# Optimization experiments

Hardware: AMD Instinct MI355X
Metric: run time of the kernel (lower is better)

Reference implementation:

```python
import jax, jax.numpy as jnp
import numpy as np

N_EXPERTS = 8
TOP_K = 2


def setup_inputs() -> dict:
    key = jax.random.key(0)
    ks = jax.random.split(key, 5)
    B, T, C, E, H = 8, 2048, 256, 8, 682  # H = int(8/3*256)
    scale = 1.0 / np.sqrt(C)
    return {
        "x": jax.random.normal(ks[0], (B, T, C), dtype=jnp.float32),
        "router_w": jax.random.normal(ks[1], (E, C), dtype=jnp.float32) * scale,
        "w1": jax.random.normal(ks[2], (E, H, C), dtype=jnp.float32) * scale,
        "w2": jax.random.normal(ks[3], (E, C, H), dtype=jnp.float32) * (1.0 / np.sqrt(H)),
        "w3": jax.random.normal(ks[4], (E, H, C), dtype=jnp.float32) * scale,
    }


def reference(x, router_w, w1, w2, w3):
    B, T, C = x.shape
    flat = x.reshape(-1, C)  # [N, C]

    # Router: softmax over experts, top-k selection, renormalize.
    logits = flat @ router_w.T                     # [N, E]
    probs = jax.nn.softmax(logits, axis=-1)
    topk_probs, topk_idx = jax.lax.top_k(probs, TOP_K)
    topk_probs = topk_probs / (jnp.sum(topk_probs, axis=-1, keepdims=True) + 1e-9)

    # Dense gate matrix [N, E]: zero for non-selected experts (same math as
    # the masked loop, since unselected experts contribute weight 0).
    onehot = jax.nn.one_hot(topk_idx, N_EXPERTS, dtype=flat.dtype)  # [N, K, E]
    gates = jnp.einsum("nk,nke->ne", topk_probs, onehot)           # [N, E]

    # SwiGLU experts, computed densely over E and combined with gates.
    h1 = jnp.einsum("nc,ehc->neh", flat, w1)       # [N, E, H]
    h3 = jnp.einsum("nc,ehc->neh", flat, w3)       # [N, E, H]
    h = jax.nn.silu(h1) * h3                       # [N, E, H]
    y = jnp.einsum("neh,ech->nec", h, w2)          # [N, E, C]
    out = jnp.einsum("ne,nec->nc", gates, y)       # [N, C]
    return out.reshape(B, T, C)
```

## Files before the change

### kernel.cpp

```cpp
#include <hip/hip_runtime.h>
#include <hip/hip_bf16.h>

#define N_TOK 16384
#define C_DIM 256
#define E_NUM 8
#define H_DIM 682
#define H_PAD 768
#define NROWS (N_TOK * 2)
#define HB 64
#define APB (NROWS / HB)
#define MAXTILE 264

typedef short short8 __attribute__((ext_vector_type(8)));
typedef float floatx4 __attribute__((ext_vector_type(4)));
typedef unsigned int uint;

__device__ inline unsigned short f2bf(float v) {
    union { float f; uint u; } x; x.f = v;
    uint r = (x.u + 0x7fffu + ((x.u >> 16) & 1u)) >> 16;
    return (unsigned short)r;
}
__device__ inline float bf2f(unsigned short v) {
    union { uint u; float f; } x; x.u = ((uint)v) << 16; return x.f;
}
__device__ inline uint pk2(float a, float b) {
    return (uint)f2bf(a) | ((uint)f2bf(b) << 16);
}

__device__ __forceinline__ void load_lds16(const void* g, void* l) {
    __builtin_amdgcn_global_load_lds(
        (const __attribute__((address_space(1))) unsigned int*)g,
        (__attribute__((address_space(3))) unsigned int*)l, 16, 0, 0);
}

#define VMCNT8 asm volatile("s_waitcnt vmcnt(8)" ::: "memory")
#define VMCNT6 asm volatile("s_waitcnt vmcnt(6)" ::: "memory")
#define VMCNT0 asm volatile("s_waitcnt vmcnt(0)" ::: "memory")
#define LGKM0  asm volatile("s_waitcnt lgkmcnt(0)" ::: "memory")

#define P13 (E_NUM * H_PAD * (C_DIM / 2))
#define P2  (E_NUM * C_DIM * (H_PAD / 2))
#define NQUAD ((2 * P13 + P2) / 4)
#define WCONV_BLKS (NQUAD / 256)
#define Q13 (P13 / 4)

__global__ __launch_bounds__(256) void prep_kernel(
    const float* __restrict__ w1, const float* __restrict__ w3, const float* __restrict__ w2,
    unsigned short* __restrict__ w1b, unsigned short* __restrict__ w3b,
    unsigned short* __restrict__ w2b,
    const float* __restrict__ x, const float* __restrict__ rw,
    unsigned short* __restrict__ xb, int* __restrict__ as_e, float* __restrict__ as_gate) {
    __shared__ float rws[E_NUM * C_DIM];
    int tid = threadIdx.x;
    if (blockIdx.x < WCONV_BLKS) {
        int q = blockIdx.x * 256 + tid;
        if (q < 2 * Q13) {
            const float* src = (q < Q13) ? w1 : w3;
            unsigned short* dst = (q < Q13) ? w1b : w3b;
            int i4 = (q < Q13) ? q : q - Q13;
            int e = i4 / (H_PAD * 32);
            int rem = i4 - e * (H_PAD * 32);
            int r = rem >> 5;
            int qc = rem & 31;
            int4 v = {0, 0, 0, 0};
            if (r < H_DIM) {
                const float* s = src + ((size_t)e * H_DIM + r) * C_DIM + qc * 8;
                float4 f0 = *(const float4*)s;
                float4 f1 = *(const float4*)(s + 4);
                v.x = pk2(f0.x, f0.y); v.y = pk2(f0.z, f0.w);
                v.z = pk2(f1.x, f1.y); v.w = pk2(f1.z, f1.w);
            }
            *(int4*)((uint*)dst + (size_t)i4 * 4) = v;
        } else {
            int i4 = q - 2 * Q13;
            int e = i4 / (C_DIM * 96);
            int rem = i4 - e * (C_DIM * 96);
            int r = rem / 96;
            int qc = rem - r * 96;
            const float* s = w2 + ((size_t)e * C_DIM + r) * H_DIM;
            int4 v = {0, 0, 0, 0};
            int j0 = qc * 4;
#pragma unroll
            for (int k = 0; k < 4; k++) {
                int j = j0 + k;
                if (j * 2 < H_DIM) {
                    float2 f = *(const float2*)(s + j * 2);
                    ((uint*)&v)[k] = pk2(f.x, f.y);
                }
            }
            *(int4*)((uint*)w2b + (size_t)i4 * 4) = v;
        }
        return;
    }
    for (int i = tid; i < E_NUM * C_DIM; i += 256) rws[i] = rw[i];
    __syncthreads();
    int wave = tid >> 6, lane = tid & 63;
    int t = (blockIdx.x - WCONV_BLKS) * 4 + wave;
    const float4 xv = *(const float4*)(x + (size_t)t * C_DIM + lane * 4);
    uint2 pk;
    pk.x = pk2(xv.x, xv.y);
    pk.y = pk2(xv.z, xv.w);
    *(uint2*)(xb + (size_t)t * C_DIM + lane * 4) = pk;
    float p[E_NUM];
#pragma unroll
    for (int e = 0; e < E_NUM; e++) {
        const float* wr = &rws[e * C_DIM + lane * 4];
        p[e] = xv.x * wr[0] + xv.y * wr[1] + xv.z * wr[2] + xv.w * wr[3];
    }
#pragma unroll
    for (int off = 32; off >= 1; off >>= 1) {
#pragma unroll
        for (int e = 0; e < E_NUM; e++) p[e] += __shfl_down(p[e], off, 64);
    }
    if (lane == 0) {
        float m = p[0];
#pragma unroll
        for (int e = 1; e < E_NUM; e++) m = fmaxf(m, p[e]);
        float s = 0.f, q[E_NUM];
#pragma unroll
        for (int e = 0; e < E_NUM; e++) { q[e] = expf(p[e] - m); s += q[e]; }
#pragma unroll
        for (int e = 0; e < E_NUM; e++) q[e] /= s;
        int e0 = 0;
#pragma unroll
        for (int e = 1; e < E_NUM; e++) if (q[e] > q[e0]) e0 = e;
        int e1 = (e0 == 0) ? 1 : 0;
#pragma unroll
        for (int e = 0; e < E_NUM; e++) {
            if (e != e0 && q[e] > q[e1]) e1 = e;
        }
        float g0 = q[e0], g1 = q[e1];
        float denom = g0 + g1 + 1e-9f;
        g0 /= denom; g1 /= denom;
        as_e[t * 2] = e0; as_gate[t * 2] = g0;
        as_e[t * 2 + 1] = e1; as_gate[t * 2 + 1] = g1;
    }
}

__global__ __launch_bounds__(256) void hist_kernel(const int* __restrict__ as_e,
                                                   int* __restrict__ block_hist) {
    __shared__ int lh[E_NUM];
    int b = blockIdx.x, tid = threadIdx.x;
    if (tid < E_NUM) lh[tid] = 0;
    __syncthreads();
    for (int i = tid; i < APB; i += 256) atomicAdd(&lh[as_e[b * APB + i]], 1);
    __syncthreads();
    if (tid < E_NUM) block_hist[b * E_NUM + tid] = lh[tid];
}

__global__ void scan2_kernel(const int* __restrict__ block_hist, int* __restrict__ offsets,
                             int* __restrict__ block_base, int* __restrict__ tile_base) {
    __shared__ int tot[E_NUM], off[E_NUM];
    int e = threadIdx.x;
    if (e < E_NUM) {
        int s = 0;
        for (int b = 0; b < HB; b++) s += block_hist[b * E_NUM + e];
        tot[e] = s;
    }
    __syncthreads();
    if (e == 0) {
        int acc = 0;
        for (int i = 0; i < E_NUM; i++) { off[i] = acc; offsets[i] = acc; acc += tot[i]; }
        offsets[E_NUM] = acc;
        int t = 0;
        tile_base[0] = 0;
        for (int i = 0; i < E_NUM; i++) { t += (tot[i] + 127) / 128; tile_base[i + 1] = t; }
    }
    __syncthreads();
    if (e < E_NUM) {
        int acc = off[e];
        for (int b = 0; b < HB; b++) { block_base[b * E_NUM + e] = acc; acc += block_hist[b * E_NUM + e]; }
    }
}

__global__ __launch_bounds__(256) void scatter_kernel(
    const int* __restrict__ as_e, const int* __restrict__ block_base,
    int* __restrict__ row_token, int* __restrict__ as_row) {
    __shared__ int cur[E_NUM];
    int b = blockIdx.x, tid = threadIdx.x;
    if (tid < E_NUM) cur[tid] = block_base[b * E_NUM + tid];
    __syncthreads();
    for (int i = tid; i < APB; i += 256) {
        int a = b * APB + i;
        int e = as_e[a];
        int p = atomicAdd(&cur[e], 1);
        row_token[p] = a >> 1;
        as_row[a] = p;
    }
}

__device__ __forceinline__ int tile_to_expert(const int* __restrict__ tile_base, int bid) {
    int e = 0;
#pragma unroll
    for (int i = 1; i < E_NUM; i++) e += (bid >= tile_base[i]) ? 1 : 0;
    return e;
}

__global__ __launch_bounds__(256, 2) void expert_ffn1(
    const unsigned short* __restrict__ xb, const unsigned short* __restrict__ w1b,
    const unsigned short* __restrict__ w3b, const int* __restrict__ offsets,
    const int* __restrict__ tile_base, const int* __restrict__ row_token,
    unsigned short* __restrict__ h) {
    int bid = blockIdx.x;
    int xcd = bid & 7;
    int local = bid >> 3;
    int tq = local / 6;
    int c = local - tq * 6;
    int t = tq * 8 + xcd;
    if (t >= tile_base[E_NUM]) return;
    int e = tile_to_expert(tile_base, t);
    int mt = t - tile_base[e];
    int off0 = offsets[e], off1 = offsets[e + 1];
    int row0 = off0 + mt * 128;
    int mval = min(128, off1 - row0);

    __shared__ union {
        unsigned short buf[2][12288];
        unsigned short Hs[128 * 136];
    } sm;

    int tid = threadIdx.x, lane = tid & 63, w = tid >> 6;
    int wm = w & 1, wn = w >> 1;
    int ra = tid >> 2;
    int acol = (((tid & 3) ^ ((ra >> 1) & 3))) * 8;
    int tok0 = row_token[row0 + min(ra, mval - 1)];
    int tok1 = row_token[row0 + min(ra + 64, mval - 1)];
    const unsigned short* a0p = xb + (size_t)tok0 * C_DIM + acol;
    const unsigned short* a1p = xb + (size_t)tok1 * C_DIM + acol;
    const unsigned short* b1p0 = w1b + ((size_t)e * H_PAD + c * 128 + ra) * C_DIM + acol;
    const unsigned short* b1p1 = b1p0 + (size_t)64 * C_DIM;
    const unsigned short* b3p0 = w3b + ((size_t)e * H_PAD + c * 128 + ra) * C_DIM + acol;
    const unsigned short* b3p1 = b3p0 + (size_t)64 * C_DIM;

    int wofs = w * 512;
    auto stage = [&](int kt, unsigned short* base) {
        int kb = kt * 32;
        load_lds16(a0p + kb, base + wofs);
        load_lds16(a1p + kb, base + 2048 + wofs);
        load_lds16(b1p0 + kb, base + 4096 + wofs);
        load_lds16(b1p1 + kb, base + 6144 + wofs);
        load_lds16(b3p0 + kb, base + 8192 + wofs);
        load_lds16(b3p1 + kb, base + 10240 + wofs);
    };

    int ko = ((lane >> 4) ^ ((lane >> 1) & 3)) * 8;
    int l15 = lane & 15;
    int arowf = wm * 64 + l15;
    int browf = wn * 64 + l15;
    int quad = lane >> 4;

    stage(0, sm.buf[0]);

    floatx4 acc1[4][4], acc3[4][4];
#pragma unroll
    for (int m = 0; m < 4; m++)
#pragma unroll
        for (int n = 0; n < 4; n++) {
            acc1[m][n] = (floatx4){0.f, 0.f, 0.f, 0.f};
            acc3[m][n] = (floatx4){0.f, 0.f, 0.f, 0.f};
        }

#pragma unroll
    for (int kt = 0; kt < 8; kt++) {
        if (kt + 1 < 8) stage(kt + 1, sm.buf[(kt + 1) & 1]);
        if (kt + 1 < 8) { VMCNT6; } else { VMCNT0; }
        __builtin_amdgcn_s_barrier();
        const unsigned short* cur = sm.buf[kt & 1];
        short8 af[4], b1f[4], b3f[4];
#pragma unroll
        for (int m = 0; m < 4; m++) af[m] = *(short8*)&cur[(arowf + m * 16) * 32 + ko];
#pragma unroll
        for (int n = 0; n < 4; n++) {
            b1f[n] = *(short8*)&cur[4096 + (browf + n * 16) * 32 + ko];
            b3f[n] = *(short8*)&cur[8192 + (browf + n * 16) * 32 + ko];
        }
        __builtin_amdgcn_s_setprio(1);
#pragma unroll
        for (int m = 0; m < 4; m++)
#pragma unroll
            for (int n = 0; n < 4; n++) {
                acc1[m][n] = __builtin_amdgcn_mfma_f32_16x16x32_bf16(af[m], b1f[n], acc1[m][n], 0, 0, 0);
                acc3[m][n] = __builtin_amdgcn_mfma_f32_16x16x32_bf16(af[m], b3f[n], acc3[m][n], 0, 0, 0);
            }
        __builtin_amdgcn_s_setprio(0);
        LGKM0;
        __builtin_amdgcn_s_barrier();
    }
    __syncthreads();

#pragma unroll
    for (int m = 0; m < 4; m++)
#pragma unroll
        for (int n = 0; n < 4; n++)
#pragma unroll
            for (int r = 0; r < 4; r++) {
                float h1 = acc1[m][n][r], h3 = acc3[m][n][r];
                float sv = h1 / (1.0f + __expf(-h1)) * h3;
                sm.Hs[(wm * 64 + m * 16 + quad * 4 + r) * 136 + wn * 64 + n * 16 + l15] = f2bf(sv);
            }
    __syncthreads();
#pragma unroll
    for (int it = 0; it < 8; it++) {
        int s = it * 256 + tid;
        int row = s >> 4, c16 = s & 15;
        if (row < mval)
            *(int4*)(h + (size_t)(row0 + row) * H_PAD + c * 128 + c16 * 8) =
                *(int4*)&sm.Hs[row * 136 + c16 * 8];
    }
}

__global__ __launch_bounds__(256, 2) void expert_ffn2(
    const unsigned short* __restrict__ h, const unsigned short* __restrict__ w2b,
    const int* __restrict__ offsets, const int* __restrict__ tile_base,
    unsigned short* __restrict__ y) {
    int bid = blockIdx.x;
    int xcd = bid & 7;
    int local = bid >> 3;
    int tq = local >> 1;
    int p = local & 1;
    int t = tq * 8 + xcd;
    if (t >= tile_base[E_NUM]) return;
    int e = tile_to_expert(tile_base, t);
    int mt = t - tile_base[e];
    int off0 = offsets[e], off1 = offsets[e + 1];
    int row0 = off0 + mt * 128;
    int mval = min(128, off1 - row0);

    __shared__ union {
        unsigned short buf[2][16384];
        unsigned short Hs[128 * 136];
    } sm;

    int tid = threadIdx.x, lane = tid & 63, w = tid >> 6;
    int wm = w & 1, wn = w >> 1;
    int ra = tid >> 2;
    int acol = (((tid & 3) ^ ((ra >> 1) & 3))) * 8;
    const unsigned short* ap0 = h + (size_t)(row0 + ra) * H_PAD + acol;
    const unsigned short* ap1 = ap0 + (size_t)64 * H_PAD;
    const unsigned short* bp0 = w2b + ((size_t)e * C_DIM + p * 128 + ra) * H_PAD + acol;
    const unsigned short* bp1 = bp0 + (size_t)64 * H_PAD;

    int wofs = w * 512;
    auto stage = [&](int kt, unsigned short* base) {
        int kb = kt * 64;
#pragma unroll
        for (int kk = 0; kk < 2; kk++) {
            int ks = kb + kk * 32;
            unsigned short* b2 = base + kk * 8192;
            load_lds16(ap0 + ks, b2 + wofs);
            load_lds16(ap1 + ks, b2 + 2048 + wofs);
            load_lds16(bp0 + ks, b2 + 4096 + wofs);
            load_lds16(bp1 + ks, b2 + 6144 + wofs);
        }
    };

    int ko = ((lane >> 4) ^ ((lane >> 1) & 3)) * 8;
    int l15 = lane & 15;
    int arowf = wm * 64 + l15;
    int browf = wn * 64 + l15;
    int quad = lane >> 4;

    stage(0, sm.buf[0]);

    floatx4 acc[4][4];
#pragma unroll
    for (int m = 0; m < 4; m++)
#pragma unroll
        for (int n = 0; n < 4; n++) acc[m][n] = (floatx4){0.f, 0.f, 0.f, 0.f};

#pragma unroll
    for (int kt = 0; kt < H_PAD / 64; kt++) {
        if (kt + 1 < H_PAD / 64) stage(kt + 1, sm.buf[(kt + 1) & 1]);
        if (kt + 1 < H_PAD / 64) { VMCNT8; } else { VMCNT0; }
        __builtin_amdgcn_s_barrier();
        const unsigned short* cur = sm.buf[kt & 1];
#pragma unroll
        for (int kk = 0; kk < 2; kk++) {
            const unsigned short* c2 = cur + kk * 8192;
            short8 af[4], bf[4];
#pragma unroll
            for (int m = 0; m < 4; m++) af[m] = *(short8*)&c2[(arowf + m * 16) * 32 + ko];
#pragma unroll
            for (int n = 0; n < 4; n++) bf[n] = *(short8*)&c2[4096 + (browf + n * 16) * 32 + ko];
            __builtin_amdgcn_s_setprio(1);
#pragma unroll
            for (int m = 0; m < 4; m++)
#pragma unroll
                for (int n = 0; n < 4; n++)
                    acc[m][n] = __builtin_amdgcn_mfma_f32_16x16x32_bf16(af[m], bf[n], acc[m][n], 0, 0, 0);
            __builtin_amdgcn_s_setprio(0);
        }
        LGKM0;
        __builtin_amdgcn_s_barrier();
    }
    __syncthreads();

#pragma unroll
    for (int m = 0; m < 4; m++)
#pragma unroll
        for (int n = 0; n < 4; n++)
#pragma unroll
            for (int r = 0; r < 4; r++)
                sm.Hs[(wm * 64 + m * 16 + quad * 4 + r) * 136 + wn * 64 + n * 16 + l15] =
                    f2bf(acc[m][n][r]);
    __syncthreads();
#pragma unroll
    for (int it = 0; it < 8; it++) {
        int s = it * 256 + tid;
        int row = s >> 4, c16 = s & 15;
        if (row < mval)
            *(int4*)(y + (size_t)(row0 + row) * C_DIM + p * 128 + c16 * 8) =
                *(int4*)&sm.Hs[row * 136 + c16 * 8];
    }
}

__global__ __launch_bounds__(256) void combine_kernel(
    const unsigned short* __restrict__ y, const int* __restrict__ as_row,
    const float* __restrict__ as_gate, float* __restrict__ out) {
    int tid = threadIdx.x, lane = tid & 63;
    int t = blockIdx.x * 4 + (tid >> 6);
    int r0 = as_row[2 * t], r1 = as_row[2 * t + 1];
    float g0 = as_gate[2 * t], g1 = as_gate[2 * t + 1];
    uint2 a = *(const uint2*)(y + (size_t)r0 * C_DIM + lane * 4);
    uint2 b = *(const uint2*)(y + (size_t)r1 * C_DIM + lane * 4);
    float4 o;
    o.x = g0 * bf2f((unsigned short)(a.x & 0xffff)) + g1 * bf2f((unsigned short)(b.x & 0xffff));
    o.y = g0 * bf2f((unsigned short)(a.x >> 16)) + g1 * bf2f((unsigned short)(b.x >> 16));
    o.z = g0 * bf2f((unsigned short)(a.y & 0xffff)) + g1 * bf2f((unsigned short)(b.y & 0xffff));
    o.w = g0 * bf2f((unsigned short)(a.y >> 16)) + g1 * bf2f((unsigned short)(b.y >> 16));
    *(float4*)(out + (size_t)t * C_DIM + lane * 4) = o;
}

extern "C" void kernel_launch(void* const* d_in, const int* in_sizes, int n_in,
                              void* d_out, int out_size, void* d_ws, size_t ws_size,
                              hipStream_t stream) {
    const float* x = (const float*)d_in[0];
    const float* rw = (const float*)d_in[1];
    const float* w1 = (const float*)d_in[2];
    const float* w2 = (const float*)d_in[3];
    const float* w3 = (const float*)d_in[4];
    float* out = (float*)d_out;

    char* ws = (char*)d_ws;
    size_t o = 0;
    auto alloc = [&](size_t bytes) {
        void* p = ws + o;
        o = (o + bytes + 255) & ~(size_t)255;
        return p;
    };
    unsigned short* xb = (unsigned short*)alloc((size_t)N_TOK * C_DIM * 2);
    unsigned short* w1b = (unsigned short*)alloc((size_t)E_NUM * H_PAD * C_DIM * 2);
    unsigned short* w3b = (unsigned short*)alloc((size_t)E_NUM * H_PAD * C_DIM * 2);
    unsigned short* w2b = (unsigned short*)alloc((size_t)E_NUM * C_DIM * H_PAD * 2);
    unsigned short* hbuf = (unsigned short*)alloc((size_t)(NROWS + 128) * H_PAD * 2);
    unsigned short* ybuf = (unsigned short*)alloc((size_t)NROWS * C_DIM * 2);
    int* offsets = (int*)alloc((E_NUM + 1) * 4);
    int* tile_base = (int*)alloc((E_NUM + 1) * 4);
    int* as_e = (int*)alloc(NROWS * 4);
    float* as_gate = (float*)alloc(NROWS * 4);
    int* row_token = (int*)alloc(NROWS * 4);
    int* as_row = (int*)alloc(NROWS * 4);
    int* block_hist = (int*)alloc(HB * E_NUM * 4);
    int* block_base = (int*)alloc(HB * E_NUM * 4);

    prep_kernel<<<WCONV_BLKS + N_TOK / 4, 256, 0, stream>>>(
        w1, w3, w2, w1b, w3b, w2b, x, rw, xb, as_e, as_gate);
    hist_kernel<<<HB, 256, 0, stream>>>(as_e, block_hist);
    scan2_kernel<<<1, 64, 0, stream>>>(block_hist, offsets, block_base, tile_base);
    scatter_kernel<<<HB, 256, 0, stream>>>(as_e, block_base, row_token, as_row);

    expert_ffn1<<<6 * MAXTILE, 256, 0, stream>>>(xb, w1b, w3b, offsets, tile_base,
                                                 row_token, hbuf);
    expert_ffn2<<<2 * MAXTILE, 256, 0, stream>>>(hbuf, w2b, offsets, tile_base, ybuf);
    combine_kernel<<<N_TOK / 4, 256, 0, stream>>>(ybuf, as_row, as_gate, out);
}
```

Baseline: 179.0 us.

## Triple-buffer LDS K-loop and split tile staging around MFMA halves

The gate/up GEMM K-loop moves from double to triple buffering, prefetching two K-tiles ahead instead of one. Each stage is split into two halves, one issued after the w1 fragment reads and one after the w1 MFMAs, so global-to-LDS copies overlap the MFMA work. The intent is to hide global load latency behind compute. In exchange, LDS use per block grows from 48 KB to 72 KB, which can lower occupancy, and each iteration gains an extra barrier.

```diff
diff --git a/kernel.cpp b/kernel.cpp
--- a/kernel.cpp
+++ b/kernel.cpp
@@ -215,7 +215,7 @@
     int mval = min(128, off1 - row0);
 
     __shared__ union {
-        unsigned short buf[2][12288];
+        unsigned short buf[3][12288];
         unsigned short Hs[128 * 136];
     } sm;
 
@@ -233,11 +233,14 @@
     const unsigned short* b3p1 = b3p0 + (size_t)64 * C_DIM;
 
     int wofs = w * 512;
-    auto stage = [&](int kt, unsigned short* base) {
+    auto stageA = [&](int kt, unsigned short* base) {
         int kb = kt * 32;
         load_lds16(a0p + kb, base + wofs);
         load_lds16(a1p + kb, base + 2048 + wofs);
         load_lds16(b1p0 + kb, base + 4096 + wofs);
+    };
+    auto stageB = [&](int kt, unsigned short* base) {
+        int kb = kt * 32;
         load_lds16(b1p1 + kb, base + 6144 + wofs);
         load_lds16(b3p0 + kb, base + 8192 + wofs);
         load_lds16(b3p1 + kb, base + 10240 + wofs);
@@ -249,7 +252,8 @@
     int browf = wn * 64 + l15;
     int quad = lane >> 4;
 
-    stage(0, sm.buf[0]);
+    stageA(0, sm.buf[0]); stageB(0, sm.buf[0]);
+    stageA(1, sm.buf[1]); stageB(1, sm.buf[1]);
 
     floatx4 acc1[4][4], acc3[4][4];
 #pragma unroll
@@ -262,28 +266,34 @@
 
 #pragma unroll
     for (int kt = 0; kt < 8; kt++) {
-        if (kt + 1 < 8) stage(kt + 1, sm.buf[(kt + 1) & 1]);
-        if (kt + 1 < 8) { VMCNT6; } else { VMCNT0; }
+        if (kt < 7) { VMCNT6; } else { VMCNT0; }
         __builtin_amdgcn_s_barrier();
-        const unsigned short* cur = sm.buf[kt & 1];
+        const unsigned short* cur = sm.buf[kt % 3];
+        unsigned short* nbuf = sm.buf[(kt + 2) % 3];
         short8 af[4], b1f[4], b3f[4];
 #pragma unroll
         for (int m = 0; m < 4; m++) af[m] = *(short8*)&cur[(arowf + m * 16) * 32 + ko];
 #pragma unroll
-        for (int n = 0; n < 4; n++) {
-            b1f[n] = *(short8*)&cur[4096 + (browf + n * 16) * 32 + ko];
-            b3f[n] = *(short8*)&cur[8192 + (browf + n * 16) * 32 + ko];
-        }
+        for (int n = 0; n < 4; n++) b1f[n] = *(short8*)&cur[4096 + (browf + n * 16) * 32 + ko];
+        if (kt + 2 < 8) stageA(kt + 2, nbuf);
+#pragma unroll
+        for (int n = 0; n < 4; n++) b3f[n] = *(short8*)&cur[8192 + (browf + n * 16) * 32 + ko];
         __builtin_amdgcn_s_setprio(1);
 #pragma unroll
         for (int m = 0; m < 4; m++)
 #pragma unroll
-            for (int n = 0; n < 4; n++) {
+            for (int n = 0; n < 4; n++)
                 acc1[m][n] = __builtin_amdgcn_mfma_f32_16x16x32_bf16(af[m], b1f[n], acc1[m][n], 0, 0, 0);
+        __builtin_amdgcn_s_setprio(0);
+        __builtin_amdgcn_s_barrier();
+        if (kt + 2 < 8) stageB(kt + 2, nbuf);
+        __builtin_amdgcn_s_setprio(1);
+#pragma unroll
+        for (int m = 0; m < 4; m++)
+#pragma unroll
+            for (int n = 0; n < 4; n++)
                 acc3[m][n] = __builtin_amdgcn_mfma_f32_16x16x32_bf16(af[m], b3f[n], acc3[m][n], 0, 0, 0);
-            }
         __builtin_amdgcn_s_setprio(0);
-        LGKM0;
         __builtin_amdgcn_s_barrier();
     }
     __syncthreads();
```

Result: no change. 176.9 us, median of 3 (-1.2%).
